# Optimization experiments

Measured on AMD Instinct MI355X. Metric: run time of the kernel, lower is better.

Reference implementation:

```python
import jax, jax.numpy as jnp
import numpy as np

STRIDE = 1
PADDING = 1


def sign_ste(w):
    # forward: 2*(w>0)-1 ; backward: identity (straight-through estimator)
    s = 2.0 * (w > 0.0).astype(w.dtype) - 1.0
    return w + jax.lax.stop_gradient(s - w)


def setup_inputs() -> dict:
    key = jax.random.key(0)
    kx, kw = jax.random.split(key)
    x = jax.random.normal(kx, (32, 256, 56, 56), dtype=jnp.float32)
    # mirror torch.rand(shape) * 0.001
    weight = jax.random.uniform(kw, (256, 256, 3, 3), dtype=jnp.float32) * 0.001
    return {"x": x, "weight": weight}


def reference(x, weight):
    # per-output-channel scaling factor: mean |w| over (in, kh, kw), detached
    scaling = jnp.mean(jnp.abs(weight), axis=(1, 2, 3), keepdims=True)  # [O,1,1,1]
    scaling = jax.lax.stop_gradient(scaling)
    binary_weights = scaling * sign_ste(weight)
    y = jax.lax.conv_general_dilated(
        x, binary_weights,
        window_strides=(STRIDE, STRIDE),
        padding=[(PADDING, PADDING), (PADDING, PADDING)],
        dimension_numbers=("NCHW", "OIHW", "NCHW"),
    )
    return y
```

## Files before the change

### kernel.cpp

```cpp
#include <hip/hip_runtime.h>
#include <stdint.h>


__global__ __launch_bounds__(256) void csum8(const float* __restrict__ x,
                                             float4* __restrict__ u8) {
    const int id  = blockIdx.x * 256 + threadIdx.x;
    const int n   = id / 6272;
    const int rem = id - n * 6272;
    const int g   = rem / 784;
    const int hw4 = rem - g * 784;
    const float4* xp =
        (const float4*)(x + (size_t)(n * 256 + g * 32) * 3136) + hw4;
    float4 s = {0.f, 0.f, 0.f, 0.f};
#pragma unroll
    for (int c = 0; c < 32; ++c) {
        float4 v = xp[c * 784];
        s.x += v.x; s.y += v.y; s.z += v.z; s.w += v.w;
    }
    u8[id] = s;
}

__global__ __launch_bounds__(256) void boxsum(const float* __restrict__ u8,
                                              float* __restrict__ T) {
    __shared__ float Us[3136];
    const int n = blockIdx.x;
    const float* base = u8 + (size_t)n * 8 * 3136;
    for (int hw = threadIdx.x; hw < 3136; hw += 256) {
        float s = 0.f;
#pragma unroll
        for (int g = 0; g < 8; ++g) s += base[g * 3136 + hw];
        Us[hw] = s;
    }
    __syncthreads();
    float* Tn = T + (size_t)n * 3136;
    for (int hw = threadIdx.x; hw < 3136; hw += 256) {
        const int h = hw / 56, w = hw - h * 56;
        float acc = 0.f;
#pragma unroll
        for (int r = -1; r <= 1; ++r) {
            const int hh = h + r;
            if (hh < 0 || hh >= 56) continue;
#pragma unroll
            for (int s2 = -1; s2 <= 1; ++s2) {
                const int ww = w + s2;
                if (ww < 0 || ww >= 56) continue;
                acc += Us[hh * 56 + ww];
            }
        }
        Tn[hw] = acc;
    }
}

__global__ __launch_bounds__(256) void wprep(const float* __restrict__ w,
                                             float* __restrict__ scale,
                                             int* __restrict__ nneg,
                                             int* __restrict__ negidx) {
    const int o = blockIdx.x, i = threadIdx.x;
    const float* wp = w + ((size_t)o * 256 + i) * 9;
    float s = 0.f;
#pragma unroll
    for (int k = 0; k < 9; ++k) {
        const float v = wp[k];
        s += fabsf(v);
        if (v <= 0.f) {
            const int slot = atomicAdd(&nneg[o], 1);
            negidx[o * 2304 + slot] = i * 9 + k;
        }
    }
#pragma unroll
    for (int off = 32; off > 0; off >>= 1) s += __shfl_down(s, off);
    __shared__ float red[4];
    if ((i & 63) == 0) red[i >> 6] = s;
    __syncthreads();
    if (i == 0) scale[o] = (red[0] + red[1] + red[2] + red[3]) * (1.0f / 2304.0f);
}

__global__ __launch_bounds__(256) void yout(const float* __restrict__ T,
                                            const float* __restrict__ scale,
                                            const int* __restrict__ nneg,
                                            const int* __restrict__ negidx,
                                            const float* __restrict__ x,
                                            float* __restrict__ out) {
    const int b = blockIdx.x;
    const int o = b & 255, n = b >> 8;
    const float sc = scale[o];
    const int nn = nneg[o];
    const float4* Tn = (const float4*)(T + (size_t)n * 3136);
    float4* op = (float4*)(out + ((size_t)n * 256 + o) * 3136);
#pragma unroll
    for (int j = 0; j < 4; ++j) {
        const int hw4 = threadIdx.x + j * 256;
        if (hw4 >= 784) break;
        float4 v = Tn[hw4];
        v.x *= sc; v.y *= sc; v.z *= sc; v.w *= sc;
        if (nn > 0) {
            const float c2 = 2.f * sc;
            for (int q = 0; q < nn; ++q) {
                const int iof = negidx[o * 2304 + q];
                const int i = iof / 9, rs = iof - i * 9;
                const int r = rs / 3 - 1, s2 = rs - (rs / 3) * 3 - 1;
                const float* xpl = x + ((size_t)n * 256 + i) * 3136;
#pragma unroll
                for (int e = 0; e < 4; ++e) {
                    const int hw = hw4 * 4 + e;
                    const int h = hw / 56 + r, ww = hw - (hw / 56) * 56 + s2;
                    const float xv = (h >= 0 && h < 56 && ww >= 0 && ww < 56)
                                         ? xpl[h * 56 + ww] : 0.f;
                    ((float*)&v)[e] -= c2 * xv;
                }
            }
        }
        op[hw4] = v;
    }
}

extern "C" void kernel_launch(void* const* d_in, const int* in_sizes, int n_in,
                              void* d_out, int out_size, void* d_ws, size_t ws_size,
                              hipStream_t stream) {
    const float* x = (const float*)d_in[0];
    const float* w = (const float*)d_in[1];
    float* out = (float*)d_out;

    char* ws = (char*)d_ws;
    size_t off = 0;
    float* u8 = (float*)(ws + off);
    off += (size_t)32 * 8 * 3136 * 4;
    float* T = (float*)(ws + off);
    off += (size_t)32 * 3136 * 4;
    float* scale = (float*)(ws + off);
    off += 256 * 4;
    int* nneg = (int*)(ws + off);
    off += 256 * 4;
    int* negidx = (int*)(ws + off);

    hipMemsetAsync(nneg, 0, 256 * sizeof(int), stream);
    csum8<<<dim3(784), 256, 0, stream>>>(x, (float4*)u8);
    wprep<<<dim3(256), 256, 0, stream>>>(w, scale, nneg, negidx);
    boxsum<<<dim3(32), 256, 0, stream>>>(u8, T);
    yout<<<dim3(8192), 256, 0, stream>>>(T, scale, nneg, negidx, x, out);
}
```

Measured before the change: 209.6 us.

## Split channel-sum and box-sum kernels into finer blocks, drop memset launch

The channel partial-sum kernel now reduces groups of 16 channels instead of 32, doubling its thread count. The box-sum kernel is split into row-strip blocks (224 blocks instead of 32) with a halo in shared memory. The nneg counter is zeroed inside wprep instead of through a separate memset. The aim is better GPU occupancy for the small prefix kernels and one fewer launch, at the cost of a larger intermediate buffer and redundant halo-row reads.

Measured after the change: 190.6 us. 1.1x faster.

```diff
diff --git a/kernel.cpp b/kernel.cpp
--- a/kernel.cpp
+++ b/kernel.cpp
@@ -2,52 +2,54 @@
 #include <stdint.h>
 
 
-__global__ __launch_bounds__(256) void csum8(const float* __restrict__ x,
-                                             float4* __restrict__ u8) {
+__global__ __launch_bounds__(256) void csum16(const float* __restrict__ x,
+                                              float4* __restrict__ u16) {
     const int id  = blockIdx.x * 256 + threadIdx.x;
-    const int n   = id / 6272;
-    const int rem = id - n * 6272;
+    const int n   = id / 12544;
+    const int rem = id - n * 12544;
     const int g   = rem / 784;
     const int hw4 = rem - g * 784;
     const float4* xp =
-        (const float4*)(x + (size_t)(n * 256 + g * 32) * 3136) + hw4;
+        (const float4*)(x + (size_t)(n * 256 + g * 16) * 3136) + hw4;
     float4 s = {0.f, 0.f, 0.f, 0.f};
 #pragma unroll
-    for (int c = 0; c < 32; ++c) {
+    for (int c = 0; c < 16; ++c) {
         float4 v = xp[c * 784];
         s.x += v.x; s.y += v.y; s.z += v.z; s.w += v.w;
     }
-    u8[id] = s;
+    u16[id] = s;
 }
 
-__global__ __launch_bounds__(256) void boxsum(const float* __restrict__ u8,
+__global__ __launch_bounds__(256) void boxsum(const float* __restrict__ u16,
                                               float* __restrict__ T) {
-    __shared__ float Us[3136];
-    const int n = blockIdx.x;
-    const float* base = u8 + (size_t)n * 8 * 3136;
-    for (int hw = threadIdx.x; hw < 3136; hw += 256) {
+    __shared__ float Us[560];
+    const int n  = blockIdx.x / 7;
+    const int h0 = (blockIdx.x - n * 7) * 8;
+    const float* base = u16 + (size_t)n * 16 * 3136;
+    for (int idx = threadIdx.x; idx < 560; idx += 256) {
+        const int lr = idx / 56, col = idx - lr * 56;
+        const int h = h0 - 1 + lr;
         float s = 0.f;
+        if (h >= 0 && h < 56) {
+            const float* bp = base + h * 56 + col;
 #pragma unroll
-        for (int g = 0; g < 8; ++g) s += base[g * 3136 + hw];
-        Us[hw] = s;
+            for (int g = 0; g < 16; ++g) s += bp[g * 3136];
+        }
+        Us[idx] = s;
     }
     __syncthreads();
     float* Tn = T + (size_t)n * 3136;
-    for (int hw = threadIdx.x; hw < 3136; hw += 256) {
-        const int h = hw / 56, w = hw - h * 56;
+    for (int idx = threadIdx.x; idx < 448; idx += 256) {
+        const int lr = idx / 56, w = idx - lr * 56;
         float acc = 0.f;
 #pragma unroll
-        for (int r = -1; r <= 1; ++r) {
-            const int hh = h + r;
-            if (hh < 0 || hh >= 56) continue;
-#pragma unroll
-            for (int s2 = -1; s2 <= 1; ++s2) {
-                const int ww = w + s2;
-                if (ww < 0 || ww >= 56) continue;
-                acc += Us[hh * 56 + ww];
-            }
+        for (int r = 0; r < 3; ++r) {
+            const float* row = Us + (lr + r) * 56;
+            if (w > 0)  acc += row[w - 1];
+            acc += row[w];
+            if (w < 55) acc += row[w + 1];
         }
-        Tn[hw] = acc;
+        Tn[(h0 + lr) * 56 + w] = acc;
     }
 }
 
@@ -56,6 +58,8 @@
                                              int* __restrict__ nneg,
                                              int* __restrict__ negidx) {
     const int o = blockIdx.x, i = threadIdx.x;
+    if (i == 0) nneg[o] = 0;
+    __syncthreads();
     const float* wp = w + ((size_t)o * 256 + i) * 9;
     float s = 0.f;
 #pragma unroll
@@ -123,8 +127,8 @@
 
     char* ws = (char*)d_ws;
     size_t off = 0;
-    float* u8 = (float*)(ws + off);
-    off += (size_t)32 * 8 * 3136 * 4;
+    float* u16 = (float*)(ws + off);
+    off += (size_t)32 * 16 * 3136 * 4;
     float* T = (float*)(ws + off);
     off += (size_t)32 * 3136 * 4;
     float* scale = (float*)(ws + off);
@@ -133,9 +137,8 @@
     off += 256 * 4;
     int* negidx = (int*)(ws + off);
 
-    hipMemsetAsync(nneg, 0, 256 * sizeof(int), stream);
-    csum8<<<dim3(784), 256, 0, stream>>>(x, (float4*)u8);
+    csum16<<<dim3(1568), 256, 0, stream>>>(x, (float4*)u16);
     wprep<<<dim3(256), 256, 0, stream>>>(w, scale, nneg, negidx);
-    boxsum<<<dim3(32), 256, 0, stream>>>(u8, T);
+    boxsum<<<dim3(224), 256, 0, stream>>>(u16, T);
     yout<<<dim3(8192), 256, 0, stream>>>(T, scale, nneg, negidx, x, out);
 }
```
